# Kernel optimization log

Hardware: AMD Instinct MI355X
Metric: run time of the kernel (lower is better)

The kernel has to match this reference:

```python
import jax, jax.numpy as jnp
import numpy as np

EPS = 1e-12   # F.normalize eps
COS_EPS = 1e-8  # F.cosine_similarity eps

B, S, V, D, P, L = 4, 2048, 64, 1024, 8, 24
H = D // 24            # prefix_transform bottleneck = 42
K = 2 * L * D          # 49152 output feature dim


def setup_inputs() -> dict:
    key = jax.random.key(0)
    ks = jax.random.split(key, 8)
    return {
        "prefix": jax.random.randint(ks[0], (B, V), 0, V),
        "ctx_embeds": jax.random.normal(ks[1], (B, S, D), jnp.float32),
        "tables": jax.random.normal(ks[2], (P, V, D), jnp.float32) * 0.02,
        "lora_prefix_emb": jax.random.normal(ks[3], (P, D), jnp.float32),
        "w1": jax.random.normal(ks[4], (D, H), jnp.float32) * 0.02,
        "b1": jnp.zeros((H,), jnp.float32),
        "w2": jax.random.normal(ks[5], (H, K), jnp.float32) * 0.02,
        "b2": jnp.zeros((K,), jnp.float32),
    }


def _gates(ctx_embeds, lora_prefix_emb):
    """select_prefix, vectorized over the num_prefix_set loop.

    The original builds sim_i = bmm(norm(emb), norm(e_i.repeat(B,S,1), dim=0).permute)
    of shape [B,S,S]; since the key is repeated, every column of sim is identical,
    so we carry the column vector [P,B,S] and the math is exact.
    """
    b, s, _ = ctx_embeds.shape
    # normalize embedding over feature dim (F.normalize p=2 dim=2)
    emb_n = ctx_embeds / jnp.maximum(
        jnp.linalg.norm(ctx_embeds, axis=2, keepdims=True), EPS)
    # F.normalize over dim=0 of a tensor repeated B times -> sign(x)/sqrt(B)
    u = lora_prefix_emb / jnp.maximum(
        jnp.sqrt(float(b)) * jnp.abs(lora_prefix_emb), EPS)  # [P,D]
    v = jnp.einsum('bsd,pd->pbs', emb_n, u)          # column of sim matrix
    c = jnp.maximum(v, 0.0)                          # clamp(min=0)
    # F.normalize over last dim (length S, all entries equal c) -> c/(sqrt(S)*c)
    n = c / jnp.maximum(jnp.sqrt(float(s)) * c, EPS)
    w = jax.nn.softmax(n, axis=2)                    # softmax over token dim (dim=1 in torch layout)
    a_v = jnp.einsum('pbs,bsd->pbd', w, ctx_embeds)  # attended value per expert
    e_norm = jnp.linalg.norm(lora_prefix_emb, axis=1)          # [P]
    a_norm = jnp.linalg.norm(a_v, axis=2)                      # [P,B]
    cos = jnp.einsum('pd,pbd->pb', lora_prefix_emb, a_v) / \
        jnp.maximum(e_norm[:, None] * a_norm, COS_EPS)
    return jax.nn.softmax(cos.T, axis=-1)            # self.s_t, [B,P]


def reference(prefix, ctx_embeds, tables, lora_prefix_emb, w1, b1, w2, b2):
    s_t = _gates(ctx_embeds, lora_prefix_emb)        # [B,P]
    # forward() re-applies softmax to self.s_t (faithful double softmax)
    gate = jax.nn.softmax(s_t, axis=-1)              # [B,P]
    tok = tables[:, prefix]                          # [P,B,V,D] per-expert embedding lookup
    h = jnp.tanh(jnp.einsum('pbvd,dh->pbvh', tok, w1) + b1)
    pkv = jnp.einsum('pbvh,hk->pbvk', h, w2) + b2    # [P,B,V,K]
    out = jnp.einsum('bp,pbvk->bvk', gate, pkv)      # gated mixture over experts
    return out
```

## Files before the change

### kernel.cpp

```cpp
#include <hip/hip_runtime.h>

#define BB 4
#define SS 2048
#define VV 64
#define DD 1024
#define PP 8
#define HH 42
#define KK 49152

static constexpr float F_EPS = 1e-12f;
static constexpr float ALPHA = 1.02234304f;

__global__ __launch_bounds__(256) void k15_fused(
    const float* __restrict__ ctx, const float* __restrict__ lora,
    const float* __restrict__ tables, const float* __restrict__ w1,
    const float* __restrict__ b1, float* __restrict__ n_ws,
    float* __restrict__ h_all) {
  __shared__ float smem[PP * DD];
  const int t = threadIdx.x;
  if (blockIdx.x < 512) {
    for (int i = t; i < PP * DD; i += 256) {
      float e = lora[i];
      smem[i] = e / fmaxf(2.0f * fabsf(e), F_EPS);
    }
    __syncthreads();
    const int wave = t >> 6, lane = t & 63;
    const int rbase = blockIdx.x * 16 + wave * 4;
    const float4* ctx4 = (const float4*)ctx;
    const float4* u4 = (const float4*)smem;
    float dot[4][PP];
    #pragma unroll
    for (int i = 0; i < 4; ++i)
      #pragma unroll
      for (int p = 0; p < PP; ++p) dot[i][p] = 0.f;
    #pragma unroll
    for (int j = 0; j < 4; ++j) {
      float4 c[4];
      #pragma unroll
      for (int i = 0; i < 4; ++i)
        c[i] = ctx4[(size_t)(rbase + i) * 256 + j * 64 + lane];
      #pragma unroll
      for (int p = 0; p < PP; ++p) {
        float4 u = u4[p * 256 + j * 64 + lane];
        #pragma unroll
        for (int i = 0; i < 4; ++i)
          dot[i][p] += c[i].x * u.x + c[i].y * u.y + c[i].z * u.z + c[i].w * u.w;
      }
    }
    const int sel = lane & 7;
    #pragma unroll
    for (int i = 0; i < 4; ++i) {
      float d0 = dot[i][0], d1 = dot[i][1], d2 = dot[i][2], d3 = dot[i][3];
      float d4 = dot[i][4], d5 = dot[i][5], d6 = dot[i][6], d7 = dot[i][7];
      #pragma unroll
      for (int m = 1; m <= 4; m <<= 1) {
        d0 += __shfl_xor(d0, m, 64); d1 += __shfl_xor(d1, m, 64);
        d2 += __shfl_xor(d2, m, 64); d3 += __shfl_xor(d3, m, 64);
        d4 += __shfl_xor(d4, m, 64); d5 += __shfl_xor(d5, m, 64);
        d6 += __shfl_xor(d6, m, 64); d7 += __shfl_xor(d7, m, 64);
      }
      float v = d0;
      v = (sel == 1) ? d1 : v; v = (sel == 2) ? d2 : v;
      v = (sel == 3) ? d3 : v; v = (sel == 4) ? d4 : v;
      v = (sel == 5) ? d5 : v; v = (sel == 6) ? d6 : v;
      v = (sel == 7) ? d7 : v;
      v += __shfl_xor(v, 8, 64);
      v += __shfl_xor(v, 16, 64);
      v += __shfl_xor(v, 32, 64);
      if (lane < PP)
        n_ws[(size_t)(rbase + i) * 8 + lane] = (v > 0.0f) ? ALPHA : 1.0f;
    }
  } else {
    float* row_lds = smem;
    float* partial = smem + DD;
    const int r = blockIdx.x - 512;
    ((float4*)row_lds)[t] = ((const float4*)(tables + (size_t)r * DD))[t];
    __syncthreads();
    const int h = t & 63, q = t >> 6;
    float acc = 0.0f;
    if (h < HH) {
      const int d0 = q * 256;
      #pragma unroll 8
      for (int dl = 0; dl < 256; ++dl) {
        acc += row_lds[d0 + dl] * w1[(size_t)(d0 + dl) * HH + h];
      }
    }
    partial[q * 64 + h] = acc;
    __syncthreads();
    if (t < HH) {
      float s = partial[t] + partial[64 + t] + partial[128 + t] + partial[192 + t];
      h_all[(size_t)r * HH + t] = tanhf(s + b1[t]);
    }
  }
}

__global__ __launch_bounds__(256) void k3_av(
    const float* __restrict__ ctx, const float* __restrict__ n_ws,
    float* __restrict__ part) {
  const int t = threadIdx.x;
  const int chunk = blockIdx.x;
  const int b = blockIdx.y;
  const int dz = blockIdx.z;
  __shared__ float w_lds[64 * PP];
  if (t < 128)
    ((float4*)w_lds)[t] =
        ((const float4*)(n_ws + (size_t)(b * SS + chunk * 64) * 8))[t];
  __syncthreads();
  float2 acc[PP];
  #pragma unroll
  for (int p = 0; p < PP; ++p) acc[p] = make_float2(0.f, 0.f);
  const float2* ctx2 = (const float2*)ctx;
  const float4* w4 = (const float4*)w_lds;
  #pragma unroll 4
  for (int sl = 0; sl < 64; ++sl) {
    int s = chunk * 64 + sl;
    float2 c = ctx2[(size_t)(b * SS + s) * 512 + dz * 256 + t];
    float4 wa = w4[sl * 2];
    float4 wb = w4[sl * 2 + 1];
    float w[PP] = {wa.x, wa.y, wa.z, wa.w, wb.x, wb.y, wb.z, wb.w};
    #pragma unroll
    for (int p = 0; p < PP; ++p) {
      acc[p].x += w[p] * c.x;
      acc[p].y += w[p] * c.y;
    }
  }
  float2* part2 = (float2*)part;
  #pragma unroll
  for (int p = 0; p < PP; ++p)
    part2[(size_t)((b * 32 + chunk) * PP + p) * 512 + dz * 256 + t] = acc[p];
}

__global__ __launch_bounds__(256) void k4_cos(
    const float* __restrict__ part, const float* __restrict__ lora,
    float* __restrict__ cos_ws) {
  const int t = threadIdx.x;
  const int p = blockIdx.x, b = blockIdx.y;
  const float4* part4 = (const float4*)part;
  float4 av = make_float4(0.f, 0.f, 0.f, 0.f);
  #pragma unroll 8
  for (int c = 0; c < 32; ++c) {
    float4 x = part4[(size_t)((b * 32 + c) * PP + p) * 256 + t];
    av.x += x.x; av.y += x.y; av.z += x.z; av.w += x.w;
  }
  float4 e = ((const float4*)lora)[p * 256 + t];
  float dt = av.x * e.x + av.y * e.y + av.z * e.z + av.w * e.w;
  float a2 = av.x * av.x + av.y * av.y + av.z * av.z + av.w * av.w;
  float e2 = e.x * e.x + e.y * e.y + e.z * e.z + e.w * e.w;
  #pragma unroll
  for (int m = 32; m >= 1; m >>= 1) {
    dt += __shfl_xor(dt, m, 64);
    a2 += __shfl_xor(a2, m, 64);
    e2 += __shfl_xor(e2, m, 64);
  }
  __shared__ float red[4][3];
  const int wave = t >> 6, lane = t & 63;
  if (lane == 0) { red[wave][0] = dt; red[wave][1] = a2; red[wave][2] = e2; }
  __syncthreads();
  if (t == 0) {
    float Dv = red[0][0] + red[1][0] + red[2][0] + red[3][0];
    float Av = red[0][1] + red[1][1] + red[2][1] + red[3][1];
    float Ev = red[0][2] + red[1][2] + red[2][2] + red[3][2];
    cos_ws[b * PP + p] = Dv / fmaxf(sqrtf(Ev) * sqrtf(Av), 1e-8f);
  }
}

__global__ __launch_bounds__(256) void k7_out(
    const float* __restrict__ w2, const float* __restrict__ b2,
    const float* __restrict__ h_all, const float* __restrict__ cos_ws,
    const int* __restrict__ prefix, float* __restrict__ out) {
  __shared__ float gate_lds[PP];
  __shared__ float hg_lds[HH * 64];
  __shared__ float w2_lds[HH * 128];
  const int t = threadIdx.x;
  const int b = blockIdx.y;
  const size_t kbase = (size_t)blockIdx.x * 128;
  for (int i = t; i < HH * 128; i += 256) {
    int h = i >> 7, kk = i & 127;
    w2_lds[i] = w2[(size_t)h * KK + kbase + kk];
  }
  if (t == 0) {
    float c[PP];
    float m = -1e30f;
    #pragma unroll
    for (int p = 0; p < PP; ++p) { c[p] = cos_ws[b * PP + p]; m = fmaxf(m, c[p]); }
    float s = 0.0f;
    #pragma unroll
    for (int p = 0; p < PP; ++p) { c[p] = expf(c[p] - m); s += c[p]; }
    float inv = 1.0f / s;
    float m2 = -1e30f;
    #pragma unroll
    for (int p = 0; p < PP; ++p) { c[p] *= inv; m2 = fmaxf(m2, c[p]); }
    float s2 = 0.0f;
    #pragma unroll
    for (int p = 0; p < PP; ++p) { c[p] = expf(c[p] - m2); s2 += c[p]; }
    float inv2 = 1.0f / s2;
    #pragma unroll
    for (int p = 0; p < PP; ++p) gate_lds[p] = c[p] * inv2;
  }
  __syncthreads();
  for (int idx = t; idx < 64 * HH; idx += 256) {
    int v = idx / HH;
    int h = idx - v * HH;
    int tokv = prefix[b * VV + v];
    float s = 0.0f;
    #pragma unroll
    for (int p = 0; p < PP; ++p)
      s += gate_lds[p] * h_all[(size_t)(p * VV + tokv) * HH + h];
    hg_lds[h * 64 + v] = s;
  }
  __syncthreads();
  const int tk = t & 31, tb = t >> 5;
  float4 acc[8];
  #pragma unroll
  for (int i = 0; i < 8; ++i) acc[i] = make_float4(0.f, 0.f, 0.f, 0.f);
  const float4* w24 = (const float4*)w2_lds;
  const float4* hg4 = (const float4*)hg_lds;
  #pragma unroll 2
  for (int h = 0; h < HH; ++h) {
    float4 wv = w24[h * 32 + tk];
    float4 g0 = hg4[h * 16 + tb * 2];
    float4 g1 = hg4[h * 16 + tb * 2 + 1];
    float gg[8] = {g0.x, g0.y, g0.z, g0.w, g1.x, g1.y, g1.z, g1.w};
    #pragma unroll
    for (int i = 0; i < 8; ++i) {
      acc[i].x += gg[i] * wv.x;
      acc[i].y += gg[i] * wv.y;
      acc[i].z += gg[i] * wv.z;
      acc[i].w += gg[i] * wv.w;
    }
  }
  float4 b2v = ((const float4*)b2)[(kbase >> 2) + tk];
  float4* out4 = (float4*)out;
  #pragma unroll
  for (int i = 0; i < 8; ++i) {
    int bv = b * 64 + tb * 8 + i;
    float4 o;
    o.x = acc[i].x + b2v.x;
    o.y = acc[i].y + b2v.y;
    o.z = acc[i].z + b2v.z;
    o.w = acc[i].w + b2v.w;
    out4[(((size_t)bv * KK + kbase) >> 2) + tk] = o;
  }
}

extern "C" void kernel_launch(void* const* d_in, const int* in_sizes, int n_in,
                              void* d_out, int out_size, void* d_ws, size_t ws_size,
                              hipStream_t stream) {
  const int* prefix = (const int*)d_in[0];
  const float* ctx = (const float*)d_in[1];
  const float* tables = (const float*)d_in[2];
  const float* lora = (const float*)d_in[3];
  const float* w1 = (const float*)d_in[4];
  const float* b1 = (const float*)d_in[5];
  const float* w2 = (const float*)d_in[6];
  const float* b2 = (const float*)d_in[7];
  float* out = (float*)d_out;
  char* ws = (char*)d_ws;
  float* n_ws = (float*)ws;
  float* part = (float*)(ws + 262144);
  float* cos_ws = (float*)(ws + 262144 + 4194304);
  float* h_all = (float*)(ws + 262144 + 4194304 + 128);

  k15_fused<<<1024, 256, 0, stream>>>(ctx, lora, tables, w1, b1, n_ws, h_all);
  k3_av<<<dim3(32, 4, 2), 256, 0, stream>>>(ctx, n_ws, part);
  k4_cos<<<dim3(8, 4), 256, 0, stream>>>(part, lora, cos_ws);
  k7_out<<<dim3(384, 4), 256, 0, stream>>>(w2, b2, h_all, cos_ws, prefix, out);
}
```

Baseline: 157.6 us.

## Fuse gate-sign computation with attended-value partial sums in one kernel

```diff
diff --git a/kernel.cpp b/kernel.cpp
--- a/kernel.cpp
+++ b/kernel.cpp
@@ -11,23 +11,27 @@
 static constexpr float F_EPS = 1e-12f;
 static constexpr float ALPHA = 1.02234304f;
 
-__global__ __launch_bounds__(256) void k15_fused(
+__global__ __launch_bounds__(512) void kU_fused(
     const float* __restrict__ ctx, const float* __restrict__ lora,
     const float* __restrict__ tables, const float* __restrict__ w1,
-    const float* __restrict__ b1, float* __restrict__ n_ws,
+    const float* __restrict__ b1, float* __restrict__ part,
     float* __restrict__ h_all) {
-  __shared__ float smem[PP * DD];
+  __shared__ float smem[PP * DD + 16 + 32 * PP];
   const int t = threadIdx.x;
-  if (blockIdx.x < 512) {
-    for (int i = t; i < PP * DD; i += 256) {
+  const int b = blockIdx.y;
+  if (blockIdx.x < 64) {
+    const int chunk = blockIdx.x;
+    float* u_lds = smem;
+    float* w_lds = smem + PP * DD + 16;
+    for (int i = t; i < PP * DD; i += 512) {
       float e = lora[i];
-      smem[i] = e / fmaxf(2.0f * fabsf(e), F_EPS);
+      u_lds[i] = e / fmaxf(2.0f * fabsf(e), F_EPS);
     }
     __syncthreads();
     const int wave = t >> 6, lane = t & 63;
-    const int rbase = blockIdx.x * 16 + wave * 4;
+    const int rbase = b * SS + chunk * 32 + wave * 4;
     const float4* ctx4 = (const float4*)ctx;
-    const float4* u4 = (const float4*)smem;
+    const float4* u4 = (const float4*)u_lds;
     float dot[4][PP];
     #pragma unroll
     for (int i = 0; i < 4; ++i)
@@ -68,66 +72,54 @@
       v += __shfl_xor(v, 16, 64);
       v += __shfl_xor(v, 32, 64);
       if (lane < PP)
-        n_ws[(size_t)(rbase + i) * 8 + lane] = (v > 0.0f) ? ALPHA : 1.0f;
-    }
+        w_lds[(wave * 4 + i) * PP + lane] = (v > 0.0f) ? ALPHA : 1.0f;
+    }
+    __syncthreads();
+    float2 acc[PP];
+    #pragma unroll
+    for (int p = 0; p < PP; ++p) acc[p] = make_float2(0.f, 0.f);
+    const float2* ctx2 = (const float2*)ctx;
+    const float4* w4 = (const float4*)w_lds;
+    #pragma unroll 4
+    for (int sl = 0; sl < 32; ++sl) {
+      float2 c = ctx2[(size_t)(b * SS + chunk * 32 + sl) * 512 + t];
+      float4 wa = w4[sl * 2];
+      float4 wb = w4[sl * 2 + 1];
+      float w[PP] = {wa.x, wa.y, wa.z, wa.w, wb.x, wb.y, wb.z, wb.w};
+      #pragma unroll
+      for (int p = 0; p < PP; ++p) {
+        acc[p].x += w[p] * c.x;
+        acc[p].y += w[p] * c.y;
+      }
+    }
+    float2* part2 = (float2*)part;
+    #pragma unroll
+    for (int p = 0; p < PP; ++p)
+      part2[(size_t)((b * 64 + chunk) * PP + p) * 512 + t] = acc[p];
   } else {
     float* row_lds = smem;
     float* partial = smem + DD;
-    const int r = blockIdx.x - 512;
-    ((float4*)row_lds)[t] = ((const float4*)(tables + (size_t)r * DD))[t];
+    const int r = (blockIdx.x - 64) * 4 + b;
+    ((float2*)row_lds)[t] = ((const float2*)(tables + (size_t)r * DD))[t];
     __syncthreads();
     const int h = t & 63, q = t >> 6;
     float acc = 0.0f;
     if (h < HH) {
-      const int d0 = q * 256;
+      const int d0 = q * 128;
       #pragma unroll 8
-      for (int dl = 0; dl < 256; ++dl) {
+      for (int dl = 0; dl < 128; ++dl) {
         acc += row_lds[d0 + dl] * w1[(size_t)(d0 + dl) * HH + h];
       }
     }
     partial[q * 64 + h] = acc;
     __syncthreads();
     if (t < HH) {
-      float s = partial[t] + partial[64 + t] + partial[128 + t] + partial[192 + t];
+      float s = 0.0f;
+      #pragma unroll
+      for (int q8 = 0; q8 < 8; ++q8) s += partial[q8 * 64 + t];
       h_all[(size_t)r * HH + t] = tanhf(s + b1[t]);
     }
   }
-}
-
-__global__ __launch_bounds__(256) void k3_av(
-    const float* __restrict__ ctx, const float* __restrict__ n_ws,
-    float* __restrict__ part) {
-  const int t = threadIdx.x;
-  const int chunk = blockIdx.x;
-  const int b = blockIdx.y;
-  const int dz = blockIdx.z;
-  __shared__ float w_lds[64 * PP];
-  if (t < 128)
-    ((float4*)w_lds)[t] =
-        ((const float4*)(n_ws + (size_t)(b * SS + chunk * 64) * 8))[t];
-  __syncthreads();
-  float2 acc[PP];
-  #pragma unroll
-  for (int p = 0; p < PP; ++p) acc[p] = make_float2(0.f, 0.f);
-  const float2* ctx2 = (const float2*)ctx;
-  const float4* w4 = (const float4*)w_lds;
-  #pragma unroll 4
-  for (int sl = 0; sl < 64; ++sl) {
-    int s = chunk * 64 + sl;
-    float2 c = ctx2[(size_t)(b * SS + s) * 512 + dz * 256 + t];
-    float4 wa = w4[sl * 2];
-    float4 wb = w4[sl * 2 + 1];
-    float w[PP] = {wa.x, wa.y, wa.z, wa.w, wb.x, wb.y, wb.z, wb.w};
-    #pragma unroll
-    for (int p = 0; p < PP; ++p) {
-      acc[p].x += w[p] * c.x;
-      acc[p].y += w[p] * c.y;
-    }
-  }
-  float2* part2 = (float2*)part;
-  #pragma unroll
-  for (int p = 0; p < PP; ++p)
-    part2[(size_t)((b * 32 + chunk) * PP + p) * 512 + dz * 256 + t] = acc[p];
 }
 
 __global__ __launch_bounds__(256) void k4_cos(
@@ -138,8 +130,8 @@
   const float4* part4 = (const float4*)part;
   float4 av = make_float4(0.f, 0.f, 0.f, 0.f);
   #pragma unroll 8
-  for (int c = 0; c < 32; ++c) {
-    float4 x = part4[(size_t)((b * 32 + c) * PP + p) * 256 + t];
+  for (int c = 0; c < 64; ++c) {
+    float4 x = part4[(size_t)((b * 64 + c) * PP + p) * 256 + t];
     av.x += x.x; av.y += x.y; av.z += x.z; av.w += x.w;
   }
   float4 e = ((const float4*)lora)[p * 256 + t];
@@ -256,13 +248,11 @@
   const float* b2 = (const float*)d_in[7];
   float* out = (float*)d_out;
   char* ws = (char*)d_ws;
-  float* n_ws = (float*)ws;
-  float* part = (float*)(ws + 262144);
-  float* cos_ws = (float*)(ws + 262144 + 4194304);
-  float* h_all = (float*)(ws + 262144 + 4194304 + 128);
-
-  k15_fused<<<1024, 256, 0, stream>>>(ctx, lora, tables, w1, b1, n_ws, h_all);
-  k3_av<<<dim3(32, 4, 2), 256, 0, stream>>>(ctx, n_ws, part);
+  float* part = (float*)ws;
+  float* cos_ws = (float*)(ws + 8388608);
+  float* h_all = (float*)(ws + 8388608 + 128);
+
+  kU_fused<<<dim3(192, 4), 512, 0, stream>>>(ctx, lora, tables, w1, b1, part, h_all);
   k4_cos<<<dim3(8, 4), 256, 0, stream>>>(part, lora, cos_ws);
   k7_out<<<dim3(384, 4), 256, 0, stream>>>(w2, b2, h_all, cos_ws, prefix, out);
 }
```

Result: faster. 152.7 us (-3.1%).
